# Performance work log

Measured on AMD Instinct MI355X. Metric: run time of the kernel, lower is better.

The kernel has to match this reference:

```python
import jax, jax.numpy as jnp
import numpy as np

N_NODES = 100000
N_EDGES = 50000
NNZ = 1600000
D_IN = 128
D_OUT = 128  # heads(8) * out_channels(16)


def setup_inputs() -> dict:
    key = jax.random.key(0)
    k1, k2, k3, k4 = jax.random.split(key, 4)
    X = jax.random.normal(k1, (N_NODES, D_IN), dtype=jnp.float32)
    W = jax.random.normal(k2, (D_IN, D_OUT), dtype=jnp.float32) * (1.0 / np.sqrt(D_IN))
    eps = jnp.zeros((1,), dtype=jnp.float32)
    vertex = jax.random.randint(k3, (NNZ,), 0, N_NODES, dtype=jnp.int32)
    edges = jax.random.randint(k4, (NNZ,), 0, N_EDGES, dtype=jnp.int32)
    return {"X": X, "W": W, "eps": eps, "vertex": vertex, "edges": edges,
            "num_edges": N_EDGES}


def reference(X, W, eps, vertex, edges, num_edges):
    N = X.shape[0]
    Xp = X @ W                                   # [N, D_OUT] linear proj (no bias)
    Xve = Xp[vertex]                             # [nnz, D_OUT] vertex -> incidence gather
    Xe = jax.ops.segment_sum(Xve, edges, num_segments=num_edges)   # [E, D_OUT] first_aggregate='sum'
    Xev = Xe[edges]                              # [nnz, D_OUT] edge -> incidence gather
    Xv = jax.ops.segment_sum(Xev, vertex, num_segments=N)          # [N, D_OUT]
    out = (1.0 + eps) * Xp + Xv                  # GIN combine with learnable eps (eps is [1], broadcasts)
    return jax.nn.gelu(out, approximate=False)   # torch F.gelu default = exact erf
```

## Files before the change

kernel.cpp:

```cpp
#include <hip/hip_runtime.h>
#include <math.h>

#define NN 100000
#define NE 50000
#define NSEG (NE + NN)
#define DD 128

#define NBE 196
#define NBV 391
#define NB  (NBE + NBV)
#define CAP_E 8960

#define NSH 8
#define CAP_E8 1280
#define CAP_V8 640
#define EOFF (NBE * NSH * CAP_E8)
#define S_INTS (EOFF + NBV * NSH * CAP_V8)

typedef short bf16x8 __attribute__((ext_vector_type(8)));
typedef float f32x4 __attribute__((ext_vector_type(4)));
typedef float v2f __attribute__((ext_vector_type(2)));

static __device__ __forceinline__ float gelu_exact(float x) {
  return 0.5f * x * (1.0f + erff(x * 0.70710678118654752f));
}

static __device__ __forceinline__ int sbase(int g, int s) {
  return (g < NBE) ? (g * NSH + s) * CAP_E8
                   : EOFF + ((g - NBE) * NSH + s) * CAP_V8;
}

static __device__ __forceinline__ void acc2(v2f& a, unsigned u) {
  union { unsigned i; float f; } lo, hi;
  lo.i = u << 16;
  hi.i = u & 0xFFFF0000u;
  v2f t;
  t.x = lo.f;
  t.y = hi.f;
  a += t;
}

static __device__ __forceinline__ void acc4(v2f* a, uint4 u) {
  acc2(a[0], u.x); acc2(a[1], u.y); acc2(a[2], u.z); acc2(a[3], u.w);
}

static __device__ __forceinline__ unsigned pack_bf16x2(float a, float b) {
  unsigned ua = __float_as_uint(a), ub = __float_as_uint(b);
  ua = (ua + 0x7FFFu + ((ua >> 16) & 1u)) >> 16;
  ub = (ub + 0x7FFFu + ((ub >> 16) & 1u)) >> 16;
  return ua | (ub << 16);
}

static __device__ __forceinline__ unsigned short bf16_rne(float a) {
  unsigned ua = __float_as_uint(a);
  ua = (ua + 0x7FFFu + ((ua >> 16) & 1u)) >> 16;
  return (unsigned short)ua;
}

static __device__ __forceinline__ void reduce4(v2f* a) {
#pragma unroll
  for (int k = 0; k < 4; ++k) {
    float x = a[k].x, y = a[k].y;
    x += __shfl_xor(x, 16); y += __shfl_xor(y, 16);
    x += __shfl_xor(x, 32); y += __shfl_xor(y, 32);
    a[k].x = x; a[k].y = y;
  }
}

__global__ __launch_bounds__(256) void k_pass1(const int* __restrict__ vertex,
                                               const int* __restrict__ edges,
                                               int* __restrict__ gcur,
                                               int* __restrict__ S, int nnz,
                                               const float* __restrict__ W,
                                               unsigned short* __restrict__ Wt) {
  const int tid = threadIdx.x;
  const int nb1 = gridDim.x - 64;
  if (blockIdx.x >= nb1) {
    int idx = (blockIdx.x - nb1) * 256 + tid;
    int k = idx >> 7, n = idx & 127;
    Wt[n * 128 + k] = bf16_rne(W[idx]);
    return;
  }
  const int sh = blockIdx.x & 7;
  __shared__ int hist[NB];
  for (int b = tid; b < NB; b += 256) hist[b] = 0;
  __syncthreads();
  const int base = blockIdx.x * 4096;
#pragma unroll
  for (int k = 0; k < 16; ++k) {
    int i = base + tid + k * 256;
    if (i < nnz) {
      atomicAdd(&hist[edges[i] >> 8], 1);
      atomicAdd(&hist[NBE + (vertex[i] >> 8)], 1);
    }
  }
  __syncthreads();
  for (int b = tid; b < NB; b += 256) {
    int c = hist[b];
    hist[b] = c ? sbase(b, sh) + atomicAdd(&gcur[b * NSH + sh], c) : 0;
  }
  __syncthreads();
#pragma unroll
  for (int k = 0; k < 16; ++k) {
    int i = base + tid + k * 256;
    if (i < nnz) {
      int e = edges[i], v = vertex[i];
      int pe = atomicAdd(&hist[e >> 8], 1);
      S[pe] = ((e & 255) << 17) | v;
      int pv = atomicAdd(&hist[NBE + (v >> 8)], 1);
      S[pv] = ((v & 255) << 17) | e;
    }
  }
}

__global__ __launch_bounds__(256) void k_pass2(const int* __restrict__ gcur,
                                               const int* __restrict__ S,
                                               int* __restrict__ LE,
                                               unsigned short* __restrict__ LV,
                                               int* __restrict__ O, int nnz) {
  __shared__ int offs[257];
  __shared__ int cur[256];
  __shared__ int scratch[CAP_E];
  __shared__ int shn[NSH];
  const int g = blockIdx.x;
  const int tid = threadIdx.x;
  int part = 0;
  for (int i = tid; i < g * NSH; i += 256) part += gcur[i];
  cur[tid] = part;
  __syncthreads();
#pragma unroll
  for (int s2 = 128; s2 > 0; s2 >>= 1) {
    if (tid < s2) cur[tid] += cur[tid + s2];
    __syncthreads();
  }
  const bool isE = g < NBE;
  const int dbase = isE ? cur[0] : cur[0] - nnz;
  __syncthreads();
  if (tid < NSH) {
    int capS = isE ? CAP_E8 : CAP_V8;
    shn[tid] = min(gcur[g * NSH + tid], capS);
  }
  for (int k = tid; k < 257; k += 256) offs[k] = 0;
  __syncthreads();

  const int s0 = isE ? (g << 8) : ((g - NBE) << 8);
  const int segN = min(256, (isE ? NE : NN) - s0);
  const int obase = isE ? s0 : NE + 1 + s0;

#pragma unroll
  for (int s = 0; s < NSH; ++s) {
    const int ss = sbase(g, s);
    const int ns = shn[s];
    for (int t = tid; t < ns; t += 256) atomicAdd(&offs[(S[ss + t] >> 17) + 1], 1);
  }
  __syncthreads();
  for (int off = 1; off < 256; off <<= 1) {
    int y = (tid >= off) ? offs[tid + 1 - off] : 0;
    __syncthreads();
    offs[tid + 1] += y;
    __syncthreads();
  }
  cur[tid] = offs[tid];
  __syncthreads();
#pragma unroll
  for (int s = 0; s < NSH; ++s) {
    const int ss = sbase(g, s);
    const int ns = shn[s];
    for (int t = tid; t < ns; t += 256) {
      int u = S[ss + t];
      int r = atomicAdd(&cur[u >> 17], 1);
      scratch[r] = u & 0x1FFFF;
    }
  }
  __syncthreads();
  int nit = 0;
#pragma unroll
  for (int s = 0; s < NSH; ++s) nit += shn[s];
  if (isE) {
    for (int t = tid; t < nit; t += 256) LE[dbase + t] = scratch[t];
  } else {
    for (int t = tid; t < nit; t += 256) LV[dbase + t] = (unsigned short)scratch[t];
  }
  for (int k = tid; k <= segN; k += 256) O[obase + k] = dbase + offs[k];
}

__global__ __launch_bounds__(256) void k_gemm(const float* __restrict__ X,
                                              const unsigned short* __restrict__ Wt,
                                              unsigned short* __restrict__ Xb2) {
  const int tid = threadIdx.x;
  const int w = tid >> 6;
  const int l = tid & 63;
  const int lm = l & 15;
  const int lk = l >> 4;
  const int R = blockIdx.x * 64 + w * 16;
  const int arow = R + lm;
  const bool rowok = arow < NN;
  const f32x4* __restrict__ X4 = (const f32x4*)X;
  const uint4* __restrict__ Wt4 = (const uint4*)Wt;

  f32x4 acc[8];
#pragma unroll
  for (int t = 0; t < 8; ++t) acc[t] = (f32x4)(0.f);

  for (int c = 0; c < 4; ++c) {
    const int k0 = c * 32 + lk * 8;
    f32x4 x0 = (f32x4)(0.f), x1 = (f32x4)(0.f);
    if (rowok) {
      x0 = __builtin_nontemporal_load(&X4[arow * 32 + (k0 >> 2)]);
      x1 = __builtin_nontemporal_load(&X4[arow * 32 + (k0 >> 2) + 1]);
    }
    union { bf16x8 v; uint4 u; } a;
    a.u.x = pack_bf16x2(x0.x, x0.y);
    a.u.y = pack_bf16x2(x0.z, x0.w);
    a.u.z = pack_bf16x2(x1.x, x1.y);
    a.u.w = pack_bf16x2(x1.z, x1.w);
#pragma unroll
    for (int t = 0; t < 8; ++t) {
      union { bf16x8 v; uint4 u; } b;
      b.u = Wt4[(t * 16 + lm) * 16 + c * 4 + lk];
      acc[t] = __builtin_amdgcn_mfma_f32_16x16x32_bf16(a.v, b.v, acc[t], 0, 0, 0);
    }
  }

  const int drow = R + lk * 4;
#pragma unroll
  for (int r = 0; r < 4; ++r) {
    const int row = drow + r;
    if (row < NN) {
#pragma unroll
      for (int t = 0; t < 8; ++t) {
        Xb2[row * 128 + t * 16 + lm] = bf16_rne(acc[t][r]);
      }
    }
  }
}

__global__ __launch_bounds__(256) void k_edge_agg(const unsigned* __restrict__ Xb2,
                                                  const int* __restrict__ O,
                                                  const int* __restrict__ LE,
                                                  unsigned* __restrict__ Xe2) {
  const int e = blockIdx.x * 4 + (threadIdx.x >> 6);
  const int lane = threadIdx.x & 63;
  const int q = lane >> 4;
  const int ql = lane & 15;
  const int start = O[e];
  const int end = O[e + 1];
  const uint4* __restrict__ P = (const uint4*)Xb2;
  v2f a[4];
#pragma unroll
  for (int k = 0; k < 4; ++k) a[k] = (v2f)(0.f);
  int j = start + q;
  for (; j + 28 < end; j += 32) {
    int i0 = LE[j];
    int i1 = LE[j + 4];
    int i2 = LE[j + 8];
    int i3 = LE[j + 12];
    int i4 = LE[j + 16];
    int i5 = LE[j + 20];
    int i6 = LE[j + 24];
    int i7 = LE[j + 28];
    uint4 u0 = P[(size_t)i0 * 16 + ql];
    uint4 u1 = P[(size_t)i1 * 16 + ql];
    uint4 u2 = P[(size_t)i2 * 16 + ql];
    uint4 u3 = P[(size_t)i3 * 16 + ql];
    uint4 u4 = P[(size_t)i4 * 16 + ql];
    uint4 u5 = P[(size_t)i5 * 16 + ql];
    uint4 u6 = P[(size_t)i6 * 16 + ql];
    uint4 u7 = P[(size_t)i7 * 16 + ql];
    acc4(a, u0); acc4(a, u1); acc4(a, u2); acc4(a, u3);
    acc4(a, u4); acc4(a, u5); acc4(a, u6); acc4(a, u7);
  }
  for (; j + 12 < end; j += 16) {
    int i0 = LE[j];
    int i1 = LE[j + 4];
    int i2 = LE[j + 8];
    int i3 = LE[j + 12];
    uint4 u0 = P[(size_t)i0 * 16 + ql];
    uint4 u1 = P[(size_t)i1 * 16 + ql];
    uint4 u2 = P[(size_t)i2 * 16 + ql];
    uint4 u3 = P[(size_t)i3 * 16 + ql];
    acc4(a, u0); acc4(a, u1); acc4(a, u2); acc4(a, u3);
  }
  if (j + 4 < end) {
    int i0 = LE[j];
    int i1 = LE[j + 4];
    uint4 u0 = P[(size_t)i0 * 16 + ql];
    uint4 u1 = P[(size_t)i1 * 16 + ql];
    acc4(a, u0); acc4(a, u1);
    j += 8;
  }
  if (j < end) {
    acc4(a, P[(size_t)LE[j] * 16 + ql]);
  }
  reduce4(a);
  v2f sel = (q == 0) ? a[0] : (q == 1) ? a[1] : (q == 2) ? a[2] : a[3];
  Xe2[e * 64 + ql * 4 + q] = pack_bf16x2(sel.x, sel.y);
}

__global__ __launch_bounds__(256) void k_vert_agg(const unsigned* __restrict__ Xe2,
                                                  const int* __restrict__ O,
                                                  const unsigned short* __restrict__ LV,
                                                  const float* __restrict__ eps,
                                                  const unsigned* __restrict__ Xb2,
                                                  float* __restrict__ out) {
  const int v = blockIdx.x * 4 + (threadIdx.x >> 6);
  const int lane = threadIdx.x & 63;
  const int q = lane >> 4;
  const int ql = lane & 15;
  const int start = O[NE + 1 + v];
  const int end = O[NE + 2 + v];
  const uint4* __restrict__ Q = (const uint4*)Xe2;
  v2f a[4];
#pragma unroll
  for (int k = 0; k < 4; ++k) a[k] = (v2f)(0.f);
  int j = start + q;
  for (; j + 12 < end; j += 16) {
    int i0 = (int)LV[j];
    int i1 = (int)LV[j + 4];
    int i2 = (int)LV[j + 8];
    int i3 = (int)LV[j + 12];
    uint4 u0 = Q[(size_t)i0 * 16 + ql];
    uint4 u1 = Q[(size_t)i1 * 16 + ql];
    uint4 u2 = Q[(size_t)i2 * 16 + ql];
    uint4 u3 = Q[(size_t)i3 * 16 + ql];
    acc4(a, u0); acc4(a, u1); acc4(a, u2); acc4(a, u3);
  }
  if (j + 4 < end) {
    int i0 = (int)LV[j];
    int i1 = (int)LV[j + 4];
    uint4 u0 = Q[(size_t)i0 * 16 + ql];
    uint4 u1 = Q[(size_t)i1 * 16 + ql];
    acc4(a, u0); acc4(a, u1);
    j += 8;
  }
  if (j < end) {
    acc4(a, Q[(size_t)LV[j] * 16 + ql]);
  }
  reduce4(a);
  v2f sel = (q == 0) ? a[0] : (q == 1) ? a[1] : (q == 2) ? a[2] : a[3];
  unsigned su = Xb2[v * 64 + ql * 4 + q];
  union { unsigned i; float f; } plo, phi;
  plo.i = su << 16;
  phi.i = su & 0xFFFF0000u;
  const float sc = 1.0f + eps[0];
  v2f x;
  x.x = gelu_exact(fmaf(sc, plo.f, sel.x));
  x.y = gelu_exact(fmaf(sc, phi.f, sel.y));
  v2f* __restrict__ P2 = (v2f*)out;
  __builtin_nontemporal_store(x, &P2[(size_t)v * 64 + ql * 4 + q]);
}

extern "C" void kernel_launch(void* const* d_in, const int* in_sizes, int n_in,
                              void* d_out, int out_size, void* d_ws, size_t ws_size,
                              hipStream_t stream) {
  const float* X = (const float*)d_in[0];
  const float* W = (const float*)d_in[1];
  const float* eps = (const float*)d_in[2];
  const int* vertex = (const int*)d_in[3];
  const int* edges = (const int*)d_in[4];
  const int nnz = in_sizes[3];

  char* ws = (char*)d_ws;
  size_t off = 0;
  auto alloc = [&](size_t bytes) -> void* {
    void* p = ws + off;
    off = (off + bytes + 255) & ~(size_t)255;
    return p;
  };
  const size_t stagingB = (size_t)S_INTS * 4;
  const size_t xbB = (size_t)NN * DD * 2;
  void* A = alloc(xbB > stagingB ? xbB : stagingB);
  int* S = (int*)A;
  unsigned short* Xb2 = (unsigned short*)A;
  unsigned* Xe2 = (unsigned*)alloc((size_t)NE * DD * 2);
  int* LE = (int*)alloc((size_t)nnz * sizeof(int));
  unsigned short* LV =
      (unsigned short*)alloc((size_t)nnz * sizeof(unsigned short));
  int* O = (int*)alloc((size_t)(NSEG + 2) * sizeof(int));
  int* gcur = (int*)alloc((size_t)NB * NSH * sizeof(int));
  unsigned short* Wt = (unsigned short*)alloc((size_t)DD * DD * 2);
  if (off > ws_size) return;

  const int nb1 = (nnz + 4095) / 4096;
  hipMemsetAsync(gcur, 0, (size_t)NB * NSH * sizeof(int), stream);
  k_pass1<<<nb1 + 64, 256, 0, stream>>>(vertex, edges, gcur, S, nnz, W, Wt);
  k_pass2<<<NB, 256, 0, stream>>>(gcur, S, LE, LV, O, nnz);
  k_gemm<<<(NN + 63) / 64, 256, 0, stream>>>(X, Wt, Xb2);
  k_edge_agg<<<NE / 4, 256, 0, stream>>>((const unsigned*)Xb2, O, LE, Xe2);
  k_vert_agg<<<NN / 4, 256, 0, stream>>>(Xe2, O, LV, eps, (const unsigned*)Xb2,
                                         (float*)d_out);
}
```

Baseline: 310.6 us.

## Fuse CSR pass2 and GEMM into one launch, stage GEMM output through LDS

The bucket-sort second pass and the bf16 projection GEMM are merged into a single kernel whose first NB blocks run the sort and whose remaining blocks run the GEMM. The two independent stages can then overlap on the GPU, and one launch boundary disappears. The staging buffer S is moved into the output buffer so it no longer aliases Xb2, which is what makes running both stages at once legal. GEMM results are written through a shared-memory tile so global stores become coalesced 16-byte writes. In exchange, the union sizes shared memory to the sort path for every block (about 38KB), which may lower occupancy for the GEMM blocks.

```diff
diff --git a/kernel.cpp b/kernel.cpp
--- a/kernel.cpp
+++ b/kernel.cpp
@@ -16,6 +16,8 @@
 #define CAP_V8 640
 #define EOFF (NBE * NSH * CAP_E8)
 #define S_INTS (EOFF + NBV * NSH * CAP_V8)
+
+#define NBG 1563
 
 typedef short bf16x8 __attribute__((ext_vector_type(8)));
 typedef float f32x4 __attribute__((ext_vector_type(4)));
@@ -113,86 +115,100 @@
   }
 }
 
-__global__ __launch_bounds__(256) void k_pass2(const int* __restrict__ gcur,
-                                               const int* __restrict__ S,
-                                               int* __restrict__ LE,
-                                               unsigned short* __restrict__ LV,
-                                               int* __restrict__ O, int nnz) {
-  __shared__ int offs[257];
-  __shared__ int cur[256];
-  __shared__ int scratch[CAP_E];
-  __shared__ int shn[NSH];
-  const int g = blockIdx.x;
+union ShU {
+  struct {
+    int offs[257];
+    int cur[256];
+    int shn[NSH];
+    int scratch[CAP_E];
+  } s;
+  struct {
+    alignas(16) unsigned short tile[4][16][136];
+  } g;
+};
+
+__global__ __launch_bounds__(256) void k_sg(const int* __restrict__ gcur,
+                                            const int* __restrict__ S,
+                                            int* __restrict__ LE,
+                                            unsigned short* __restrict__ LV,
+                                            int* __restrict__ O, int nnz,
+                                            const float* __restrict__ X,
+                                            const unsigned short* __restrict__ Wt,
+                                            unsigned short* __restrict__ Xb2) {
+  __shared__ ShU sh;
   const int tid = threadIdx.x;
-  int part = 0;
-  for (int i = tid; i < g * NSH; i += 256) part += gcur[i];
-  cur[tid] = part;
-  __syncthreads();
-#pragma unroll
-  for (int s2 = 128; s2 > 0; s2 >>= 1) {
-    if (tid < s2) cur[tid] += cur[tid + s2];
-    __syncthreads();
-  }
-  const bool isE = g < NBE;
-  const int dbase = isE ? cur[0] : cur[0] - nnz;
-  __syncthreads();
-  if (tid < NSH) {
-    int capS = isE ? CAP_E8 : CAP_V8;
-    shn[tid] = min(gcur[g * NSH + tid], capS);
-  }
-  for (int k = tid; k < 257; k += 256) offs[k] = 0;
-  __syncthreads();
-
-  const int s0 = isE ? (g << 8) : ((g - NBE) << 8);
-  const int segN = min(256, (isE ? NE : NN) - s0);
-  const int obase = isE ? s0 : NE + 1 + s0;
-
-#pragma unroll
-  for (int s = 0; s < NSH; ++s) {
-    const int ss = sbase(g, s);
-    const int ns = shn[s];
-    for (int t = tid; t < ns; t += 256) atomicAdd(&offs[(S[ss + t] >> 17) + 1], 1);
-  }
-  __syncthreads();
-  for (int off = 1; off < 256; off <<= 1) {
-    int y = (tid >= off) ? offs[tid + 1 - off] : 0;
-    __syncthreads();
-    offs[tid + 1] += y;
-    __syncthreads();
-  }
-  cur[tid] = offs[tid];
-  __syncthreads();
-#pragma unroll
-  for (int s = 0; s < NSH; ++s) {
-    const int ss = sbase(g, s);
-    const int ns = shn[s];
-    for (int t = tid; t < ns; t += 256) {
-      int u = S[ss + t];
-      int r = atomicAdd(&cur[u >> 17], 1);
-      scratch[r] = u & 0x1FFFF;
-    }
-  }
-  __syncthreads();
-  int nit = 0;
-#pragma unroll
-  for (int s = 0; s < NSH; ++s) nit += shn[s];
-  if (isE) {
-    for (int t = tid; t < nit; t += 256) LE[dbase + t] = scratch[t];
-  } else {
-    for (int t = tid; t < nit; t += 256) LV[dbase + t] = (unsigned short)scratch[t];
-  }
-  for (int k = tid; k <= segN; k += 256) O[obase + k] = dbase + offs[k];
-}
-
-__global__ __launch_bounds__(256) void k_gemm(const float* __restrict__ X,
-                                              const unsigned short* __restrict__ Wt,
-                                              unsigned short* __restrict__ Xb2) {
-  const int tid = threadIdx.x;
+
+  if (blockIdx.x < NB) {
+    const int g = blockIdx.x;
+    int part = 0;
+    for (int i = tid; i < g * NSH; i += 256) part += gcur[i];
+    sh.s.cur[tid] = part;
+    __syncthreads();
+#pragma unroll
+    for (int s2 = 128; s2 > 0; s2 >>= 1) {
+      if (tid < s2) sh.s.cur[tid] += sh.s.cur[tid + s2];
+      __syncthreads();
+    }
+    const bool isE = g < NBE;
+    const int dbase = isE ? sh.s.cur[0] : sh.s.cur[0] - nnz;
+    __syncthreads();
+    if (tid < NSH) {
+      int capS = isE ? CAP_E8 : CAP_V8;
+      sh.s.shn[tid] = min(gcur[g * NSH + tid], capS);
+    }
+    for (int k = tid; k < 257; k += 256) sh.s.offs[k] = 0;
+    __syncthreads();
+
+    const int s0 = isE ? (g << 8) : ((g - NBE) << 8);
+    const int segN = min(256, (isE ? NE : NN) - s0);
+    const int obase = isE ? s0 : NE + 1 + s0;
+
+#pragma unroll
+    for (int s = 0; s < NSH; ++s) {
+      const int ss = sbase(g, s);
+      const int ns = sh.s.shn[s];
+      for (int t = tid; t < ns; t += 256)
+        atomicAdd(&sh.s.offs[(S[ss + t] >> 17) + 1], 1);
+    }
+    __syncthreads();
+    for (int off = 1; off < 256; off <<= 1) {
+      int y = (tid >= off) ? sh.s.offs[tid + 1 - off] : 0;
+      __syncthreads();
+      sh.s.offs[tid + 1] += y;
+      __syncthreads();
+    }
+    sh.s.cur[tid] = sh.s.offs[tid];
+    __syncthreads();
+#pragma unroll
+    for (int s = 0; s < NSH; ++s) {
+      const int ss = sbase(g, s);
+      const int ns = sh.s.shn[s];
+      for (int t = tid; t < ns; t += 256) {
+        int u = S[ss + t];
+        int r = atomicAdd(&sh.s.cur[u >> 17], 1);
+        sh.s.scratch[r] = u & 0x1FFFF;
+      }
+    }
+    __syncthreads();
+    int nit = 0;
+#pragma unroll
+    for (int s = 0; s < NSH; ++s) nit += sh.s.shn[s];
+    if (isE) {
+      for (int t = tid; t < nit; t += 256) LE[dbase + t] = sh.s.scratch[t];
+    } else {
+      for (int t = tid; t < nit; t += 256)
+        LV[dbase + t] = (unsigned short)sh.s.scratch[t];
+    }
+    for (int k = tid; k <= segN; k += 256) O[obase + k] = dbase + sh.s.offs[k];
+    return;
+  }
+
+  const int bg = blockIdx.x - NB;
   const int w = tid >> 6;
   const int l = tid & 63;
   const int lm = l & 15;
   const int lk = l >> 4;
-  const int R = blockIdx.x * 64 + w * 16;
+  const int R = bg * 64 + w * 16;
   const int arow = R + lm;
   const bool rowok = arow < NN;
   const f32x4* __restrict__ X4 = (const f32x4*)X;
@@ -222,15 +238,23 @@
     }
   }
 
-  const int drow = R + lk * 4;
 #pragma unroll
   for (int r = 0; r < 4; ++r) {
-    const int row = drow + r;
-    if (row < NN) {
-#pragma unroll
-      for (int t = 0; t < 8; ++t) {
-        Xb2[row * 128 + t * 16 + lm] = bf16_rne(acc[t][r]);
-      }
+#pragma unroll
+    for (int t = 0; t < 8; ++t) {
+      sh.g.tile[w][lk * 4 + r][t * 16 + lm] = bf16_rne(acc[t][r]);
+    }
+  }
+  uint4* __restrict__ Xb2q = (uint4*)Xb2;
+#pragma unroll
+  for (int i = 0; i < 4; ++i) {
+    const int u = i * 64 + l;
+    const int row16 = u >> 4;
+    const int chunk = u & 15;
+    const int grow = R + row16;
+    if (grow < NN) {
+      uint4 val = *(const uint4*)&sh.g.tile[w][row16][chunk * 8];
+      Xb2q[(size_t)grow * 16 + chunk] = val;
     }
   }
 }
@@ -367,11 +391,9 @@
     off = (off + bytes + 255) & ~(size_t)255;
     return p;
   };
-  const size_t stagingB = (size_t)S_INTS * 4;
-  const size_t xbB = (size_t)NN * DD * 2;
-  void* A = alloc(xbB > stagingB ? xbB : stagingB);
-  int* S = (int*)A;
-  unsigned short* Xb2 = (unsigned short*)A;
+  int* S = (int*)d_out;
+  unsigned short* Xb2 =
+      (unsigned short*)alloc((size_t)NN * DD * 2);
   unsigned* Xe2 = (unsigned*)alloc((size_t)NE * DD * 2);
   int* LE = (int*)alloc((size_t)nnz * sizeof(int));
   unsigned short* LV =
@@ -384,8 +406,7 @@
   const int nb1 = (nnz + 4095) / 4096;
   hipMemsetAsync(gcur, 0, (size_t)NB * NSH * sizeof(int), stream);
   k_pass1<<<nb1 + 64, 256, 0, stream>>>(vertex, edges, gcur, S, nnz, W, Wt);
-  k_pass2<<<NB, 256, 0, stream>>>(gcur, S, LE, LV, O, nnz);
-  k_gemm<<<(NN + 63) / 64, 256, 0, stream>>>(X, Wt, Xb2);
+  k_sg<<<NB + NBG, 256, 0, stream>>>(gcur, S, LE, LV, O, nnz, X, Wt, Xb2);
   k_edge_agg<<<NE / 4, 256, 0, stream>>>((const unsigned*)Xb2, O, LE, Xe2);
   k_vert_agg<<<NN / 4, 256, 0, stream>>>(Xe2, O, LV, eps, (const unsigned*)Xb2,
                                          (float*)d_out);
```

Result: faster. 295.3 us (-4.9%).
